# Kernel tuning notes

Measured on AMD Instinct MI355X. Metric: run time of the kernel, lower is better.

The kernel has to match this reference:

```python
import jax, jax.numpy as jnp
import numpy as np
from jax import lax

B, S, C_IN, D, H, P, W, DFF, K = 32, 4096, 32, 256, 8, 24, 64, 512, 5
DH = D // H
EPS = 1e-5


def _make_starts():
    stride = max(1, W // 2)
    idx = list(range(0, max(S - W + 1, 1), stride))
    if len(idx) == 0 or idx[-1] != S - W:
        if S - W >= 0:
            idx.append(S - W)
    return np.asarray(idx)

STARTS = _make_starts()                      # [M]
WIDX = STARTS[:, None] + np.arange(W)        # [M, W] patch gather indices


def setup_inputs() -> dict:
    key = jax.random.key(0)
    ks = jax.random.split(key, 24)
    r = lambda i, shape, s=0.02: (jax.random.normal(ks[i], shape, jnp.float32) * s)
    return {
        "x": jax.random.normal(ks[0], (B, S, C_IN), jnp.float32),
        "last_close_unused": jnp.zeros((B,), jnp.float32),
        "dw_w": r(1, (C_IN, 1, K), 0.2),      # depthwise conv kernel
        "pw_w": r(2, (D, C_IN), 0.1),         # pointwise conv (1x1)
        "bn_g": jnp.ones((D,), jnp.float32),
        "bn_b": jnp.zeros((D,), jnp.float32),
        "lg_Wq": r(3, (D, D)), "lg_Wk": r(4, (D, D)),
        "lg_Wv": r(5, (D, D)), "lg_Wo": r(6, (D, D)),
        "dec_Qd": r(7, (P, D), 1.0 / np.sqrt(D)),
        "dec_Wq": r(8, (D, D)), "dec_Wk": r(9, (D, D)),
        "dec_Wv": r(10, (D, D)), "dec_Wo": r(11, (D, D)),
        "ff1_w": r(12, (DFF, D)), "ff1_b": jnp.zeros((DFF,), jnp.float32),
        "ff2_w": r(13, (D, DFF)), "ff2_b": jnp.zeros((D,), jnp.float32),
        "out_w": r(14, (1, D)), "out_b": jnp.zeros((1,), jnp.float32),
        "gate_logits": jnp.tile(jnp.array([0.2, 0.4, 0.4], jnp.float32), (P, 1)),
    }


def _ln(x):
    m = x.mean(-1, keepdims=True)
    v = ((x - m) ** 2).mean(-1, keepdims=True)
    return (x - m) / jnp.sqrt(v + EPS)


def _split(t):  # [B, L, D] -> [B, H, L, DH]
    return t.reshape(t.shape[0], -1, H, DH).transpose(0, 2, 1, 3)


def _mha(Q, KV, Wq, Wk, Wv, scale):
    q = _split(Q @ Wq.T)
    k = _split(KV @ Wk.T)
    v = _split(KV @ Wv.T)
    attn = jax.nn.softmax(jnp.einsum('bhqd,bhkd->bhqk', q, k) * scale, axis=-1)
    o = jnp.einsum('bhqk,bhkd->bhqd', attn, v)
    o = o.transpose(0, 2, 1, 3).reshape(Q.shape[0], -1, D)
    return o, attn


def reference(x, last_close_unused, dw_w, pw_w, bn_g, bn_b,
              lg_Wq, lg_Wk, lg_Wv, lg_Wo,
              dec_Qd, dec_Wq, dec_Wk, dec_Wv, dec_Wo,
              ff1_w, ff1_b, ff2_w, ff2_b, out_w, out_b, gate_logits):
    # --- DepthwisePointwise front-end ---
    xt = jnp.transpose(x, (0, 2, 1))                         # [B, C, S]
    z = lax.conv_general_dilated(xt, dw_w, (1,), [(K // 2, K // 2)],
                                 dimension_numbers=('NCH', 'OIH', 'NCH'),
                                 feature_group_count=C_IN)
    z = jnp.einsum('dc,bcs->bds', pw_w, z)                   # pointwise 1x1
    z = jax.nn.gelu(z, approximate=False)
    m = z.mean((0, 2), keepdims=True)                        # BatchNorm1d (batch stats)
    v = ((z - m) ** 2).mean((0, 2), keepdims=True)
    z = (z - m) / jnp.sqrt(v + EPS) * bn_g[None, :, None] + bn_b[None, :, None]
    z = jnp.transpose(z, (0, 2, 1))                          # [B, S, D]

    # --- LocalGlobalAttention: patch-mean queries over full sequence K/V ---
    Q = z[:, WIDX].mean(axis=2)                              # [B, M, D]
    scale = 1.0 / np.sqrt(DH)
    o, attn_g = _mha(Q, z, lg_Wq, lg_Wk, lg_Wv, scale)
    Hh = _ln(o @ lg_Wo.T + Q)                                # [B, M, D]

    # --- CrossDecoder: learned queries ---
    Qd = jnp.broadcast_to(dec_Qd[None], (B, P, D))
    o2, attn_d = _mha(Qd, Hh, dec_Wq, dec_Wk, dec_Wv, scale)
    z2 = _ln(o2 @ dec_Wo.T + Qd)
    u = jax.nn.gelu(z2 @ ff1_w.T + ff1_b, approximate=False)
    u = _ln(u @ ff2_w.T + ff2_b + z2)
    y_global = (u @ out_w.T + out_b)[..., 0]                 # [B, P]

    # --- Gated combine: residual=0, local=global ---
    g = jax.nn.softmax(gate_logits, axis=-1)                 # [P, 3]
    y = g[:, 1][None, :] * y_global + g[:, 2][None, :] * y_global
    return (y, attn_g, attn_d)
```

## Files before the change

kernel.cpp:

```cpp
#include <hip/hip_runtime.h>
#include <hip/hip_bf16.h>

typedef unsigned short u16;
typedef __attribute__((ext_vector_type(4))) float f32x4;
typedef __attribute__((ext_vector_type(8))) short s16x8;

__device__ __forceinline__ float b2f(u16 u) { return __uint_as_float(((unsigned)u) << 16); }
__device__ __forceinline__ u16 f2b(float f) {
    unsigned u = __float_as_uint(f);
    unsigned r = (u + 0x7fffu + ((u >> 16) & 1u)) >> 16;
    return (u16)r;
}
__device__ __forceinline__ float gelu_f(float x) {
    return 0.5f * x * (1.0f + erff(x * 0.70710678118654752f));
}

__global__ __launch_bounds__(256) void dw_k(const float* __restrict__ x,
        const float* __restrict__ dw_w, u16* __restrict__ z1b)
{
    int g = blockIdx.x * 256 + threadIdx.x;
    int c = g & 31, grp = g >> 5;
    int b = grp >> 9, s8 = (grp & 511) << 3;
    float wv[5];
    #pragma unroll
    for (int k = 0; k < 5; ++k) wv[k] = dw_w[c * 5 + k];
    const float* xb = x + ((size_t)b * 4096 + s8) * 32 + c;
    float xv[12];
    #pragma unroll
    for (int i = 0; i < 12; ++i) {
        int s = s8 + i - 2;
        xv[i] = (s >= 0 && s < 4096) ? xb[(i - 2) * 32] : 0.0f;
    }
    u16* zb = z1b + ((size_t)b * 4096 + s8) * 32 + c;
    #pragma unroll
    for (int j = 0; j < 8; ++j) {
        float acc = 0;
        #pragma unroll
        for (int k = 0; k < 5; ++k) acc += xv[j + k] * wv[k];
        zb[j * 32] = f2b(acc);
    }
}

__global__ __launch_bounds__(256) void prep0_k(const float* __restrict__ pw_w,
        const float* __restrict__ lg_Wq, const float* __restrict__ lg_Wo,
        const float* __restrict__ dec_Wk, const float* __restrict__ dec_Wv,
        const float* __restrict__ dec_Wo, const float* __restrict__ ff1_w,
        const float* __restrict__ ff2_w,
        u16* __restrict__ pwb, u16* __restrict__ Wq_b, u16* __restrict__ Wo_b,
        u16* __restrict__ Wk2_b, u16* __restrict__ Wv2_b, u16* __restrict__ Wo2b,
        u16* __restrict__ ff1b, u16* __restrict__ ff2b)
{
    int idx = blockIdx.x * 256 + threadIdx.x;
    if (idx < 327680) {
        int which = idx >> 16, r = idx & 65535;
        const float* srcs[5] = {lg_Wq, lg_Wo, dec_Wk, dec_Wv, dec_Wo};
        u16* dsts[5] = {Wq_b, Wo_b, Wk2_b, Wv2_b, Wo2b};
        dsts[which][r] = f2b(srcs[which][r]);
    } else if (idx < 458752) {
        int r = idx - 327680;
        ff1b[r] = f2b(ff1_w[r]);
    } else if (idx < 589824) {
        int r = idx - 458752;
        ff2b[r] = f2b(ff2_w[r]);
    } else {
        int r = idx - 589824;
        pwb[r] = f2b(pw_w[r]);
    }
}

__global__ __launch_bounds__(256) void pw_k(const u16* __restrict__ z1b,
        const u16* __restrict__ pwb, u16* __restrict__ zp,
        float* __restrict__ csum, float* __restrict__ csum2)
{
    __shared__ u16 As[64][32];
    const int t = threadIdx.x;
    const int r0 = blockIdx.x * 64;
    const int lane = t & 63, w = t >> 6;
    const int l16 = lane & 15, hi = lane >> 4;

    {
        int row = t >> 2, seg = t & 3;
        *(s16x8*)&As[row][seg * 8] = *(const s16x8*)(z1b + (size_t)(r0 + row) * 32 + seg * 8);
    }
    __syncthreads();

    const int n0 = w * 64;
    f32x4 zero = {0, 0, 0, 0};
    s16x8 bf[4];
    #pragma unroll
    for (int ni = 0; ni < 4; ++ni)
        bf[ni] = *(const s16x8*)(pwb + (n0 + ni * 16 + l16) * 32 + hi * 8);

    float cl[4] = {0,0,0,0}, ch[4] = {0,0,0,0};
    float ql[4] = {0,0,0,0}, qh[4] = {0,0,0,0};

    #pragma unroll
    for (int mi = 0; mi < 4; ++mi) {
        s16x8 af = *(const s16x8*)&As[mi * 16 + l16][hi * 8];
        #pragma unroll
        for (int ni = 0; ni < 4; ++ni) {
            f32x4 acc = __builtin_amdgcn_mfma_f32_16x16x32_bf16(af, bf[ni], zero, 0, 0, 0);
            int col = n0 + ni * 16 + l16;
            int rowb = r0 + mi * 16 + hi * 4;
            #pragma unroll
            for (int r = 0; r < 4; ++r) {
                float e = gelu_f(acc[r]);
                zp[(size_t)(rowb + r) * 256 + col] = f2b(e);
                if (mi < 2) { cl[ni] += e; ql[ni] += e * e; }
                else        { ch[ni] += e; qh[ni] += e * e; }
            }
        }
    }
    #pragma unroll
    for (int ni = 0; ni < 4; ++ni) {
        #pragma unroll
        for (int m = 16; m <= 32; m <<= 1) {
            cl[ni] += __shfl_xor(cl[ni], m);
            ch[ni] += __shfl_xor(ch[ni], m);
            ql[ni] += __shfl_xor(ql[ni], m);
            qh[ni] += __shfl_xor(qh[ni], m);
        }
        if (lane < 16) {
            int col = n0 + ni * 16 + lane;
            size_t bc = (size_t)(r0 >> 5);
            csum [bc * 256 + col]       = cl[ni];
            csum [(bc + 1) * 256 + col] = ch[ni];
            csum2[bc * 256 + col]       = ql[ni];
            csum2[(bc + 1) * 256 + col] = qh[ni];
        }
    }
}

__global__ __launch_bounds__(256) void stats2_k(const float* __restrict__ csum,
        const float* __restrict__ csum2, float* __restrict__ statp)
{
    int j = blockIdx.x, t = threadIdx.x;
    float s1 = 0, s2 = 0;
    for (int i = 0; i < 64; ++i) {
        s1 += csum [(size_t)(j * 64 + i) * 256 + t];
        s2 += csum2[(size_t)(j * 64 + i) * 256 + t];
    }
    statp[j * 512 + t] = s1;
    statp[j * 512 + 256 + t] = s2;
}

__global__ __launch_bounds__(256) void prep1_k(const float* __restrict__ statp,
        const float* __restrict__ bn_g, const float* __restrict__ bn_b,
        const float* __restrict__ gate_logits,
        float* __restrict__ a_ws, float* __restrict__ c_ws, float* __restrict__ coef)
{
    int t = threadIdx.x;
    float s1 = 0, s2 = 0;
    for (int j = 0; j < 64; ++j) {
        s1 += statp[j * 512 + t];
        s2 += statp[j * 512 + 256 + t];
    }
    const float invN = 1.0f / 131072.0f;
    float mean = s1 * invN;
    float var = s2 * invN - mean * mean;
    float av = bn_g[t] * rsqrtf(var + 1e-5f);
    a_ws[t] = av;
    c_ws[t] = bn_b[t] - mean * av;
    if (t < 24) {
        float g0 = gate_logits[t * 3], g1 = gate_logits[t * 3 + 1], g2 = gate_logits[t * 3 + 2];
        float mx = fmaxf(g0, fmaxf(g1, g2));
        float e0 = __expf(g0 - mx), e1 = __expf(g1 - mx), e2 = __expf(g2 - mx);
        coef[t] = (e1 + e2) / (e0 + e1 + e2);
    }
}

__global__ __launch_bounds__(256) void prep2b_k(const float* __restrict__ lg_Wk,
        const float* __restrict__ lg_Wv, const float* __restrict__ a_ws,
        const float* __restrict__ c_ws,
        u16* __restrict__ Wk_b, u16* __restrict__ Wv_b,
        float* __restrict__ betak, float* __restrict__ betav)
{
    __shared__ float red[4];
    int bid = blockIdx.x;
    int which = bid >> 8, row = bid & 255, t = threadIdx.x;
    const float* Wsrc = which ? lg_Wv : lg_Wk;
    float wv = Wsrc[row * 256 + t];
    (which ? Wv_b : Wk_b)[row * 256 + t] = f2b(wv * a_ws[t]);
    float v = wv * c_ws[t];
    for (int m = 32; m; m >>= 1) v += __shfl_xor(v, m);
    if ((t & 63) == 0) red[t >> 6] = v;
    __syncthreads();
    if (t == 0) (which ? betav : betak)[row] = red[0] + red[1] + red[2] + red[3];
}

__global__ __launch_bounds__(256) void q2_k(const float* __restrict__ dec_Qd,
        const float* __restrict__ dec_Wq, float* __restrict__ q2)
{
    __shared__ float wq[16][260];
    __shared__ float qd[24][260];
    int j = blockIdx.x, t = threadIdx.x;
    for (int idx = t; idx < 4096; idx += 256) {
        int tl = idx >> 8, d = idx & 255;
        wq[tl][d] = dec_Wq[(j * 16 + tl) * 256 + d];
    }
    for (int idx = t; idx < 6144; idx += 256) {
        int p = idx >> 8, d = idx & 255;
        qd[p][d] = dec_Qd[idx];
    }
    __syncthreads();
    for (int o = t; o < 384; o += 256) {
        int p = o >> 4, tl = o & 15;
        float s = 0;
        #pragma unroll 8
        for (int d = 0; d < 256; ++d) s += qd[p][d] * wq[tl][d];
        q2[p * 256 + j * 16 + tl] = s;
    }
}

__global__ __launch_bounds__(256) void qfinal_k(const float* __restrict__ csum,
        const float* __restrict__ a_ws, const float* __restrict__ c_ws,
        float* __restrict__ Qf, u16* __restrict__ Qb)
{
    int bid = blockIdx.x;
    int m = bid & 127, t = threadIdx.x;
    float val = 0.0f;
    if (m < 127) {
        float c0 = csum[(size_t)bid * 256 + t];
        float c1 = csum[(size_t)(bid + 1) * 256 + t];
        val = (c0 + c1) * (1.0f / 64.0f) * a_ws[t] + c_ws[t];
    }
    Qf[(size_t)bid * 256 + t] = val;
    Qb[(size_t)bid * 256 + t] = f2b(val);
}

__global__ __launch_bounds__(256) void kv_k(const u16* __restrict__ zp,
        const u16* __restrict__ Wk, const u16* __restrict__ Wv,
        const float* __restrict__ betak, const float* __restrict__ betav,
        u16* __restrict__ kb, u16* __restrict__ vT)
{
    __shared__ u16 As[64 * 256];
    const int t = threadIdx.x;
    const int r0 = blockIdx.x * 64;
    const int lane = t & 63, w = t >> 6;
    const int l16 = lane & 15, hi = lane >> 4;

    const u16* Ag = zp + (size_t)r0 * 256;
    #pragma unroll
    for (int i = 0; i < 8; ++i) {
        int c = t + i * 256;
        int row = c >> 5, c16 = c & 31;
        s16x8 v = *(const s16x8*)(Ag + row * 256 + c16 * 8);
        int boff = (c16 * 16) ^ ((row & 7) << 4);
        *(s16x8*)((char*)As + row * 512 + boff) = v;
    }
    __syncthreads();

    const int n0 = w * 64;
    f32x4 zero = {0, 0, 0, 0};
    f32x4 acc[4][4];
    #pragma unroll
    for (int mi = 0; mi < 4; ++mi)
        #pragma unroll
        for (int ni = 0; ni < 4; ++ni) acc[mi][ni] = zero;

    #pragma unroll
    for (int kk = 0; kk < 8; ++kk) {
        s16x8 af[4], bfk[4];
        #pragma unroll
        for (int mi = 0; mi < 4; ++mi) {
            int row = mi * 16 + l16;
            int boff = (kk * 64 + hi * 16) ^ ((row & 7) << 4);
            af[mi] = *(const s16x8*)((const char*)As + row * 512 + boff);
        }
        #pragma unroll
        for (int ni = 0; ni < 4; ++ni)
            bfk[ni] = *(const s16x8*)(Wk + (n0 + ni * 16 + l16) * 256 + kk * 32 + hi * 8);
        #pragma unroll
        for (int mi = 0; mi < 4; ++mi)
            #pragma unroll
            for (int ni = 0; ni < 4; ++ni)
                acc[mi][ni] = __builtin_amdgcn_mfma_f32_16x16x32_bf16(af[mi], bfk[ni], acc[mi][ni], 0, 0, 0);
    }
    #pragma unroll
    for (int mi = 0; mi < 4; ++mi) {
        #pragma unroll
        for (int ni = 0; ni < 4; ++ni) {
            int col = n0 + ni * 16 + l16;
            float bv = betak[col];
            int rowb = r0 + mi * 16 + hi * 4;
            #pragma unroll
            for (int r = 0; r < 4; ++r)
                kb[(size_t)(rowb + r) * 256 + col] = f2b(acc[mi][ni][r] + bv);
        }
    }
    #pragma unroll
    for (int mi = 0; mi < 4; ++mi)
        #pragma unroll
        for (int ni = 0; ni < 4; ++ni) acc[mi][ni] = zero;
    #pragma unroll
    for (int kk = 0; kk < 8; ++kk) {
        s16x8 af[4], bfv[4];
        #pragma unroll
        for (int mi = 0; mi < 4; ++mi) {
            int row = mi * 16 + l16;
            int boff = (kk * 64 + hi * 16) ^ ((row & 7) << 4);
            af[mi] = *(const s16x8*)((const char*)As + row * 512 + boff);
        }
        #pragma unroll
        for (int ni = 0; ni < 4; ++ni)
            bfv[ni] = *(const s16x8*)(Wv + (n0 + ni * 16 + l16) * 256 + kk * 32 + hi * 8);
        #pragma unroll
        for (int mi = 0; mi < 4; ++mi)
            #pragma unroll
            for (int ni = 0; ni < 4; ++ni)
                acc[mi][ni] = __builtin_amdgcn_mfma_f32_16x16x32_bf16(af[mi], bfv[ni], acc[mi][ni], 0, 0, 0);
    }
    const int b = r0 >> 12, sbase = r0 & 4095;
    #pragma unroll
    for (int mi = 0; mi < 4; ++mi) {
        #pragma unroll
        for (int ni = 0; ni < 4; ++ni) {
            int col = n0 + ni * 16 + l16;
            float bv = betav[col];
            int h = col >> 5, dh = col & 31;
            int s = sbase + mi * 16 + hi * 4;
            ushort4 pk;
            pk.x = f2b(acc[mi][ni][0] + bv);
            pk.y = f2b(acc[mi][ni][1] + bv);
            pk.z = f2b(acc[mi][ni][2] + bv);
            pk.w = f2b(acc[mi][ni][3] + bv);
            *(ushort4*)(vT + ((size_t)((b * 8 + h) * 32 + dh)) * 4096 + s) = pk;
        }
    }
}

template<int MODE>
__global__ __launch_bounds__(256) void gemm_g(const u16* __restrict__ A,
        const u16* __restrict__ W, const float* __restrict__ bias,
        void* __restrict__ Cout, int K, int ntn)
{
    __shared__ u16 As[64 * 256];
    const int t = threadIdx.x;
    const int rt = blockIdx.x / ntn, nt = blockIdx.x % ntn;
    const int r0 = rt * 64, N = ntn * 256;
    const int lane = t & 63, w = t >> 6;
    const int l16 = lane & 15, hi = lane >> 4;

    const u16* Ag = A + (size_t)r0 * K;
    const int n0 = w * 64;
    f32x4 zero = {0, 0, 0, 0};
    f32x4 acc[4][4];
    #pragma unroll
    for (int mi = 0; mi < 4; ++mi)
        #pragma unroll
        for (int ni = 0; ni < 4; ++ni) acc[mi][ni] = zero;

    for (int kc = 0; kc < K; kc += 256) {
        if (kc) __syncthreads();
        #pragma unroll
        for (int i = 0; i < 8; ++i) {
            int c = t + i * 256;
            int row = c >> 5, c16 = c & 31;
            s16x8 v = *(const s16x8*)(Ag + (size_t)row * K + kc + c16 * 8);
            int boff = (c16 * 16) ^ ((row & 7) << 4);
            *(s16x8*)((char*)As + row * 512 + boff) = v;
        }
        __syncthreads();
        #pragma unroll
        for (int kk = 0; kk < 8; ++kk) {
            s16x8 af[4], bf[4];
            #pragma unroll
            for (int mi = 0; mi < 4; ++mi) {
                int row = mi * 16 + l16;
                int boff = (kk * 64 + hi * 16) ^ ((row & 7) << 4);
                af[mi] = *(const s16x8*)((const char*)As + row * 512 + boff);
            }
            #pragma unroll
            for (int ni = 0; ni < 4; ++ni) {
                int j = nt * 256 + n0 + ni * 16 + l16;
                bf[ni] = *(const s16x8*)(W + (size_t)j * K + kc + kk * 32 + hi * 8);
            }
            #pragma unroll
            for (int mi = 0; mi < 4; ++mi)
                #pragma unroll
                for (int ni = 0; ni < 4; ++ni)
                    acc[mi][ni] = __builtin_amdgcn_mfma_f32_16x16x32_bf16(af[mi], bf[ni], acc[mi][ni], 0, 0, 0);
        }
    }

    #pragma unroll
    for (int mi = 0; mi < 4; ++mi) {
        #pragma unroll
        for (int ni = 0; ni < 4; ++ni) {
            int col = nt * 256 + n0 + ni * 16 + l16;
            float bv = bias ? bias[col] : 0.0f;
            int rowb = r0 + mi * 16 + hi * 4;
            #pragma unroll
            for (int r = 0; r < 4; ++r) {
                float v = acc[mi][ni][r] + bv;
                if (MODE == 0)      ((u16*)Cout)[(size_t)(rowb + r) * N + col] = f2b(v);
                else if (MODE == 1) ((float*)Cout)[(size_t)(rowb + r) * N + col] = v;
                else                ((u16*)Cout)[(size_t)(rowb + r) * N + col] = f2b(gelu_f(v));
            }
        }
    }
}

__global__ __launch_bounds__(512) void attn_p1(const u16* __restrict__ qb,
        const u16* __restrict__ kb, const u16* __restrict__ vT,
        float* __restrict__ den, float* __restrict__ o_part)
{
    const int bid = blockIdx.x;
    const int b = bid >> 6, h = (bid >> 3) & 7, chunk = bid & 7;
    const int t = threadIdx.x, w = t >> 6, lane = t & 63;
    const int l16 = lane & 15, hi = lane >> 4;
    const float scale = 0.17677669529663687f;

    __shared__ u16 p_lds[8][16][48];

    s16x8 qf = *(const s16x8*)(qb + ((size_t)(b * 128 + w * 16 + l16)) * 256 + h * 32 + hi * 8);
    const u16* kbase = kb + (size_t)b * 4096 * 256 + h * 32 + hi * 8;
    const u16* vbase = vT + ((size_t)(b * 8 + h)) * 32 * 4096 + hi * 8;

    float dacc[4] = {0, 0, 0, 0};
    f32x4 zero = {0, 0, 0, 0};
    f32x4 oacc[2]; oacc[0] = zero; oacc[1] = zero;

    const int sbeg = chunk * 512, send = sbeg + 512;
    for (int s0 = sbeg; s0 < send; s0 += 32) {
        #pragma unroll
        for (int sub = 0; sub < 2; ++sub) {
            int sg = s0 + sub * 16 + l16;
            s16x8 kf = *(const s16x8*)(kbase + (size_t)sg * 256);
            f32x4 lg = __builtin_amdgcn_mfma_f32_16x16x32_bf16(qf, kf, zero, 0, 0, 0);
            #pragma unroll
            for (int r = 0; r < 4; ++r) {
                float e = __expf(lg[r] * scale);
                dacc[r] += e;
                p_lds[w][hi * 4 + r][sub * 16 + l16] = f2b(e);
            }
        }
        s16x8 pf = *(const s16x8*)(&p_lds[w][l16][hi * 8]);
        #pragma unroll
        for (int vi = 0; vi < 2; ++vi) {
            s16x8 vf = *(const s16x8*)(vbase + ((size_t)(vi * 16 + l16)) * 4096 + s0);
            oacc[vi] = __builtin_amdgcn_mfma_f32_16x16x32_bf16(pf, vf, oacc[vi], 0, 0, 0);
        }
    }

    #pragma unroll
    for (int m = 1; m <= 8; m <<= 1) {
        #pragma unroll
        for (int r = 0; r < 4; ++r) dacc[r] += __shfl_xor(dacc[r], m);
    }
    if (l16 == 0) {
        #pragma unroll
        for (int r = 0; r < 4; ++r)
            den[(size_t)chunk * 32768 + (b * 8 + h) * 128 + w * 16 + hi * 4 + r] = dacc[r];
    }
    #pragma unroll
    for (int vi = 0; vi < 2; ++vi) {
        #pragma unroll
        for (int r = 0; r < 4; ++r) {
            int mg = w * 16 + hi * 4 + r;
            o_part[(size_t)chunk * 1048576 + (size_t)(b * 128 + mg) * 256 + h * 32 + vi * 16 + l16] = oacc[vi][r];
        }
    }
}

__global__ __launch_bounds__(256) void dinv_k(const float* __restrict__ den, float* __restrict__ den_inv)
{
    int i = blockIdx.x * 256 + threadIdx.x;
    float s = 0;
    #pragma unroll
    for (int c = 0; c < 8; ++c) s += den[(size_t)c * 32768 + i];
    den_inv[i] = 1.0f / s;
}

__global__ __launch_bounds__(256) void norm_k(const float* __restrict__ o_part,
        const float* __restrict__ den_inv, u16* __restrict__ ob)
{
    size_t idx = (size_t)blockIdx.x * 256 + threadIdx.x;
    int row = (int)(idx >> 8);
    int col = (int)(idx & 255);
    int b = row >> 7, m = row & 127, h = col >> 5;
    float s = 0;
    #pragma unroll
    for (int c = 0; c < 8; ++c) s += o_part[(size_t)c * 1048576 + idx];
    ob[idx] = f2b(s * den_inv[b * 1024 + h * 128 + m]);
}

__global__ __launch_bounds__(512) void attn_p2(const u16* __restrict__ qb,
        const u16* __restrict__ kb, const float* __restrict__ den_inv,
        float* __restrict__ attn_out)
{
    const int bid = blockIdx.x;
    const int b = bid >> 6, h = (bid >> 3) & 7, chunk = bid & 7;
    const int t = threadIdx.x, w = t >> 6, lane = t & 63;
    const int l16 = lane & 15, hi = lane >> 4;
    const float scale = 0.17677669529663687f;

    __shared__ float buf[8][16][68];

    s16x8 qf = *(const s16x8*)(qb + ((size_t)(b * 128 + w * 16 + l16)) * 256 + h * 32 + hi * 8);
    const u16* kbase = kb + (size_t)b * 4096 * 256 + h * 32 + hi * 8;

    float rinv[4];
    #pragma unroll
    for (int r = 0; r < 4; ++r)
        rinv[r] = den_inv[b * 1024 + h * 128 + w * 16 + hi * 4 + r];

    f32x4 zero = {0, 0, 0, 0};
    float* ab = attn_out + (size_t)(b * 8 + h) * 127 * 4096;
    const int nrow = (w < 7) ? 16 : 15;

    const int sbeg = chunk * 512, send = sbeg + 512;
    for (int s0 = sbeg; s0 < send; s0 += 64) {
        #pragma unroll
        for (int kk = 0; kk < 4; ++kk) {
            int sg = s0 + kk * 16 + l16;
            s16x8 kf = *(const s16x8*)(kbase + (size_t)sg * 256);
            f32x4 lg = __builtin_amdgcn_mfma_f32_16x16x32_bf16(qf, kf, zero, 0, 0, 0);
            #pragma unroll
            for (int r = 0; r < 4; ++r)
                buf[w][hi * 4 + r][kk * 16 + l16] = __expf(lg[r] * scale) * rinv[r];
        }
        float* dst = ab + (size_t)(w * 16) * 4096 + s0 + lane;
        for (int r = 0; r < nrow; ++r)
            dst[(size_t)r * 4096] = buf[w][r][lane];
    }
}

__global__ __launch_bounds__(256) void ln_hh(const float* __restrict__ og,
        const float* __restrict__ Qf, u16* __restrict__ Hb)
{
    __shared__ float red[8];
    int row = blockIdx.x, t = threadIdx.x;
    float v = og[(size_t)row * 256 + t] + Qf[(size_t)row * 256 + t];
    float s = v;
    for (int m = 32; m; m >>= 1) s += __shfl_xor(s, m);
    if ((t & 63) == 0) red[t >> 6] = s;
    __syncthreads();
    float mean = (red[0] + red[1] + red[2] + red[3]) * (1.0f / 256.0f);
    __syncthreads();
    float d = v - mean;
    float q = d * d;
    for (int m = 32; m; m >>= 1) q += __shfl_xor(q, m);
    if ((t & 63) == 0) red[t >> 6] = q;
    __syncthreads();
    float var = (red[0] + red[1] + red[2] + red[3]) * (1.0f / 256.0f);
    Hb[(size_t)row * 256 + t] = f2b(d * rsqrtf(var + 1e-5f));
}

__global__ __launch_bounds__(256) void dec_attn_k(const float* __restrict__ q2,
        const u16* __restrict__ k2b, const u16* __restrict__ v2b,
        float* __restrict__ attn_d, u16* __restrict__ o2b)
{
    __shared__ float qs2[24 * 32];
    __shared__ float ks[128][33];
    __shared__ float vs[128][33];
    __shared__ float lg2[24 * 128];
    __shared__ float sinv[24];
    int bid = blockIdx.x, b = bid >> 3, h = bid & 7;
    int t = threadIdx.x;
    const float scale = 0.17677669529663687f;
    for (int idx = t; idx < 4096; idx += 256) {
        int row = idx >> 5, c = idx & 31;
        ks[row][c] = b2f(k2b[((size_t)(b * 128 + row)) * 256 + h * 32 + c]);
        vs[row][c] = b2f(v2b[((size_t)(b * 128 + row)) * 256 + h * 32 + c]);
    }
    for (int idx = t; idx < 768; idx += 256) {
        int p = idx >> 5, i = idx & 31;
        qs2[idx] = q2[p * 256 + h * 32 + i];
    }
    __syncthreads();
    for (int idx = t; idx < 3048; idx += 256) {
        int p = idx / 127, m = idx - p * 127;
        float s = 0;
        #pragma unroll 8
        for (int i = 0; i < 32; ++i) s += qs2[p * 32 + i] * ks[m][i];
        lg2[p * 128 + m] = __expf(s * scale);
    }
    __syncthreads();
    if (t < 24) {
        float s = 0;
        for (int m = 0; m < 127; ++m) s += lg2[t * 128 + m];
        sinv[t] = 1.0f / s;
    }
    __syncthreads();
    float* ad = attn_d + (size_t)bid * 24 * 127;
    for (int idx = t; idx < 3048; idx += 256) {
        int p = idx / 127, m = idx - p * 127;
        float av = lg2[p * 128 + m] * sinv[p];
        lg2[p * 128 + m] = av;
        ad[idx] = av;
    }
    __syncthreads();
    for (int idx = t; idx < 768; idx += 256) {
        int p = idx >> 5, dh = idx & 31;
        float s = 0;
        for (int m = 0; m < 127; ++m)
            s += lg2[p * 128 + m] * vs[m][dh];
        o2b[((size_t)(b * 24 + p)) * 256 + h * 32 + dh] = f2b(s);
    }
}

__global__ __launch_bounds__(256) void ln3_k(const float* __restrict__ og2,
        const float* __restrict__ dec_Qd, float* __restrict__ z2f, u16* __restrict__ z2b)
{
    __shared__ float red[8];
    int row = blockIdx.x, p = row % 24, t = threadIdx.x;
    float v = og2[(size_t)row * 256 + t] + dec_Qd[p * 256 + t];
    float s = v;
    for (int m = 32; m; m >>= 1) s += __shfl_xor(s, m);
    if ((t & 63) == 0) red[t >> 6] = s;
    __syncthreads();
    float mean = (red[0] + red[1] + red[2] + red[3]) * (1.0f / 256.0f);
    __syncthreads();
    float d = v - mean, q = d * d;
    for (int m = 32; m; m >>= 1) q += __shfl_xor(q, m);
    if ((t & 63) == 0) red[t >> 6] = q;
    __syncthreads();
    float var = (red[0] + red[1] + red[2] + red[3]) * (1.0f / 256.0f);
    float u = d * rsqrtf(var + 1e-5f);
    z2f[(size_t)row * 256 + t] = u;
    z2b[(size_t)row * 256 + t] = f2b(u);
}

__global__ __launch_bounds__(256) void ln5_k(const float* __restrict__ uraw,
        const float* __restrict__ z2f, const float* __restrict__ out_w,
        const float* __restrict__ out_b, const float* __restrict__ coef,
        float* __restrict__ y)
{
    __shared__ float red[8];
    int row = blockIdx.x, p = row % 24, t = threadIdx.x;
    float v = uraw[(size_t)row * 256 + t] + z2f[(size_t)row * 256 + t];
    float s = v;
    for (int m = 32; m; m >>= 1) s += __shfl_xor(s, m);
    if ((t & 63) == 0) red[t >> 6] = s;
    __syncthreads();
    float mean = (red[0] + red[1] + red[2] + red[3]) * (1.0f / 256.0f);
    __syncthreads();
    float d = v - mean, q = d * d;
    for (int m = 32; m; m >>= 1) q += __shfl_xor(q, m);
    if ((t & 63) == 0) red[t >> 6] = q;
    __syncthreads();
    float var = (red[0] + red[1] + red[2] + red[3]) * (1.0f / 256.0f);
    float u = d * rsqrtf(var + 1e-5f);
    __syncthreads();
    float yp = u * out_w[t];
    for (int m = 32; m; m >>= 1) yp += __shfl_xor(yp, m);
    if ((t & 63) == 0) red[t >> 6] = yp;
    __syncthreads();
    if (t == 0) {
        float tot = red[0] + red[1] + red[2] + red[3] + out_b[0];
        y[row] = coef[p] * tot;
    }
}

extern "C" void kernel_launch(void* const* d_in, const int* in_sizes, int n_in,
                              void* d_out, int out_size, void* d_ws, size_t ws_size,
                              hipStream_t stream)
{
    const float* x        = (const float*)d_in[0];
    const float* dw_w     = (const float*)d_in[2];
    const float* pw_w     = (const float*)d_in[3];
    const float* bn_g     = (const float*)d_in[4];
    const float* bn_b     = (const float*)d_in[5];
    const float* lg_Wq    = (const float*)d_in[6];
    const float* lg_Wk    = (const float*)d_in[7];
    const float* lg_Wv    = (const float*)d_in[8];
    const float* lg_Wo    = (const float*)d_in[9];
    const float* dec_Qd   = (const float*)d_in[10];
    const float* dec_Wq   = (const float*)d_in[11];
    const float* dec_Wk   = (const float*)d_in[12];
    const float* dec_Wv   = (const float*)d_in[13];
    const float* dec_Wo   = (const float*)d_in[14];
    const float* ff1_w    = (const float*)d_in[15];
    const float* ff1_b    = (const float*)d_in[16];
    const float* ff2_w    = (const float*)d_in[17];
    const float* ff2_b    = (const float*)d_in[18];
    const float* out_w    = (const float*)d_in[19];
    const float* out_b    = (const float*)d_in[20];
    const float* gate_lg  = (const float*)d_in[21];

    char* ws = (char*)d_ws;
    size_t off = 0;
    auto alloc = [&](size_t bytes) -> void* {
        void* p = ws + off;
        off = (off + bytes + 255) & ~(size_t)255;
        return p;
    };
    u16*   zp    = (u16*)  alloc(67108864);
    u16*   kb    = (u16*)  alloc(67108864);
    u16*   vT    = (u16*)  alloc(67108864);
    u16*   z1b   = (u16*)  alloc(8388608);
    float* csum  = (float*)alloc(4194304);
    float* csum2 = (float*)alloc(4194304);
    float* Qf    = (float*)alloc(4194304);
    u16*   Qb    = (u16*)  alloc(2097152);
    u16*   qb    = (u16*)  alloc(2097152);
    u16*   ob    = (u16*)  alloc(2097152);
    float* og    = (float*)alloc(4194304);
    u16*   Hb    = (u16*)  alloc(2097152);
    u16*   k2b   = (u16*)  alloc(2097152);
    u16*   v2b   = (u16*)  alloc(2097152);
    float* o_part= (float*)alloc(33554432);
    u16*   o2b   = (u16*)  alloc(393216);
    float* og2   = (float*)alloc(786432);
    float* z2f   = (float*)alloc(786432);
    u16*   z2b   = (u16*)  alloc(393216);
    u16*   u1b   = (u16*)  alloc(786432);
    float* uraw  = (float*)alloc(786432);
    float* q2    = (float*)alloc(24576);
    float* den   = (float*)alloc(1048576);
    float* den_i = (float*)alloc(131072);
    float* statp = (float*)alloc(131072);
    float* a_ws  = (float*)alloc(1024);
    float* c_ws  = (float*)alloc(1024);
    float* betak = (float*)alloc(1024);
    float* betav = (float*)alloc(1024);
    float* coef  = (float*)alloc(256);
    u16*   pwb   = (u16*)  alloc(16384);
    u16*   Wk_b  = (u16*)  alloc(131072);
    u16*   Wv_b  = (u16*)  alloc(131072);
    u16*   Wq_b  = (u16*)  alloc(131072);
    u16*   Wo_b  = (u16*)  alloc(131072);
    u16*   Wk2_b = (u16*)  alloc(131072);
    u16*   Wv2_b = (u16*)  alloc(131072);
    u16*   Wo2b  = (u16*)  alloc(131072);
    u16*   ff1b  = (u16*)  alloc(262144);
    u16*   ff2b  = (u16*)  alloc(262144);

    float* y_out  = (float*)d_out;
    float* attn_g = y_out + 768;
    float* attn_d = attn_g + (size_t)32 * 8 * 127 * 4096;

    dw_k<<<2048, 256, 0, stream>>>(x, dw_w, z1b);
    prep0_k<<<2336, 256, 0, stream>>>(pw_w, lg_Wq, lg_Wo, dec_Wk, dec_Wv, dec_Wo, ff1_w, ff2_w,
                                      pwb, Wq_b, Wo_b, Wk2_b, Wv2_b, Wo2b, ff1b, ff2b);
    pw_k<<<2048, 256, 0, stream>>>(z1b, pwb, zp, csum, csum2);
    stats2_k<<<64, 256, 0, stream>>>(csum, csum2, statp);
    prep1_k<<<1, 256, 0, stream>>>(statp, bn_g, bn_b, gate_lg, a_ws, c_ws, coef);
    prep2b_k<<<512, 256, 0, stream>>>(lg_Wk, lg_Wv, a_ws, c_ws, Wk_b, Wv_b, betak, betav);
    q2_k<<<16, 256, 0, stream>>>(dec_Qd, dec_Wq, q2);
    qfinal_k<<<4096, 256, 0, stream>>>(csum, a_ws, c_ws, Qf, Qb);
    kv_k<<<2048, 256, 0, stream>>>(zp, Wk_b, Wv_b, betak, betav, kb, vT);
    gemm_g<0><<<64, 256, 0, stream>>>(Qb, Wq_b, nullptr, qb, 256, 1);
    attn_p1<<<2048, 512, 0, stream>>>(qb, kb, vT, den, o_part);
    dinv_k<<<128, 256, 0, stream>>>(den, den_i);
    norm_k<<<4096, 256, 0, stream>>>(o_part, den_i, ob);
    attn_p2<<<2048, 512, 0, stream>>>(qb, kb, den_i, attn_g);
    gemm_g<1><<<64, 256, 0, stream>>>(ob, Wo_b, nullptr, og, 256, 1);
    ln_hh<<<4096, 256, 0, stream>>>(og, Qf, Hb);
    gemm_g<0><<<64, 256, 0, stream>>>(Hb, Wk2_b, nullptr, k2b, 256, 1);
    gemm_g<0><<<64, 256, 0, stream>>>(Hb, Wv2_b, nullptr, v2b, 256, 1);
    dec_attn_k<<<256, 256, 0, stream>>>(q2, k2b, v2b, attn_d, o2b);
    gemm_g<1><<<12, 256, 0, stream>>>(o2b, Wo2b, nullptr, og2, 256, 1);
    ln3_k<<<768, 256, 0, stream>>>(og2, dec_Qd, z2f, z2b);
    gemm_g<2><<<24, 256, 0, stream>>>(z2b, ff1b, ff1_b, u1b, 256, 2);
    gemm_g<1><<<12, 256, 0, stream>>>(u1b, ff2b, ff2_b, uraw, 512, 1);
    ln5_k<<<768, 256, 0, stream>>>(uraw, z2f, out_w, out_b, coef, y_out);
}
```

Before: 560.7 us.

## Fuse depthwise into pointwise conv, fuse Q build into Q GEMM, prefetch attention K/V

Merges the depthwise conv into the pointwise conv kernel via a shared-memory halo tile, which drops the z1b intermediate buffer. It also folds the patch-mean Q construction into the Q projection GEMM with the softmax scale times log2(e) pre-applied, so attention can use exp2f. Other changes: the Q residual is recomputed inside ln_hh, the K2/V2 GEMMs are merged into one launch, and the attention loop software-prefetches the next K/V fragments. The goal is fewer launches and less intermediate traffic, at the cost of rounding Q to bf16 with the scale already folded in.

New measurement: 554.6 us, median of 2. Within noise of the previous version (-1.1%).

```diff
diff --git a/kernel.cpp b/kernel.cpp
--- a/kernel.cpp
+++ b/kernel.cpp
@@ -1,5 +1,6 @@
 #include <hip/hip_runtime.h>
 #include <hip/hip_bf16.h>
+#include <cmath>
 
 typedef unsigned short u16;
 typedef __attribute__((ext_vector_type(4))) float f32x4;
@@ -15,31 +16,7 @@
     return 0.5f * x * (1.0f + erff(x * 0.70710678118654752f));
 }
 
-__global__ __launch_bounds__(256) void dw_k(const float* __restrict__ x,
-        const float* __restrict__ dw_w, u16* __restrict__ z1b)
-{
-    int g = blockIdx.x * 256 + threadIdx.x;
-    int c = g & 31, grp = g >> 5;
-    int b = grp >> 9, s8 = (grp & 511) << 3;
-    float wv[5];
-    #pragma unroll
-    for (int k = 0; k < 5; ++k) wv[k] = dw_w[c * 5 + k];
-    const float* xb = x + ((size_t)b * 4096 + s8) * 32 + c;
-    float xv[12];
-    #pragma unroll
-    for (int i = 0; i < 12; ++i) {
-        int s = s8 + i - 2;
-        xv[i] = (s >= 0 && s < 4096) ? xb[(i - 2) * 32] : 0.0f;
-    }
-    u16* zb = z1b + ((size_t)b * 4096 + s8) * 32 + c;
-    #pragma unroll
-    for (int j = 0; j < 8; ++j) {
-        float acc = 0;
-        #pragma unroll
-        for (int k = 0; k < 5; ++k) acc += xv[j + k] * wv[k];
-        zb[j * 32] = f2b(acc);
-    }
-}
+#define FOLD 0.25503590f
 
 __global__ __launch_bounds__(256) void prep0_k(const float* __restrict__ pw_w,
         const float* __restrict__ lg_Wq, const float* __restrict__ lg_Wo,
@@ -68,19 +45,35 @@
     }
 }
 
-__global__ __launch_bounds__(256) void pw_k(const u16* __restrict__ z1b,
-        const u16* __restrict__ pwb, u16* __restrict__ zp,
-        float* __restrict__ csum, float* __restrict__ csum2)
-{
-    __shared__ u16 As[64][32];
+__global__ __launch_bounds__(256) void dwpw_k(const float* __restrict__ x,
+        const float* __restrict__ dw_w, const u16* __restrict__ pwb,
+        u16* __restrict__ zp, float* __restrict__ csum, float* __restrict__ csum2)
+{
+    __shared__ float xs[68][33];
+    __shared__ __align__(16) u16 As[64][40];
     const int t = threadIdx.x;
+    const int b = blockIdx.x >> 6, s0 = (blockIdx.x & 63) << 6;
     const int r0 = blockIdx.x * 64;
     const int lane = t & 63, w = t >> 6;
     const int l16 = lane & 15, hi = lane >> 4;
 
-    {
-        int row = t >> 2, seg = t & 3;
-        *(s16x8*)&As[row][seg * 8] = *(const s16x8*)(z1b + (size_t)(r0 + row) * 32 + seg * 8);
+    for (int idx = t; idx < 68 * 32; idx += 256) {
+        int row = idx >> 5, c = idx & 31;
+        int sg = s0 - 2 + row;
+        xs[row][c] = (sg >= 0 && sg < 4096) ? x[((size_t)b * 4096 + sg) * 32 + c] : 0.0f;
+    }
+    const int cc = t & 31;
+    float wv[5];
+    #pragma unroll
+    for (int k = 0; k < 5; ++k) wv[k] = dw_w[cc * 5 + k];
+    __syncthreads();
+    #pragma unroll
+    for (int i = 0; i < 8; ++i) {
+        int sl = (t + i * 256) >> 5;
+        float acc = 0;
+        #pragma unroll
+        for (int k = 0; k < 5; ++k) acc += xs[sl + k][cc] * wv[k];
+        As[sl][cc] = f2b(acc);
     }
     __syncthreads();
 
@@ -212,20 +205,81 @@
     }
 }
 
-__global__ __launch_bounds__(256) void qfinal_k(const float* __restrict__ csum,
+__global__ __launch_bounds__(256) void qgemm_k(const float* __restrict__ csum,
         const float* __restrict__ a_ws, const float* __restrict__ c_ws,
-        float* __restrict__ Qf, u16* __restrict__ Qb)
-{
-    int bid = blockIdx.x;
-    int m = bid & 127, t = threadIdx.x;
-    float val = 0.0f;
-    if (m < 127) {
-        float c0 = csum[(size_t)bid * 256 + t];
-        float c1 = csum[(size_t)(bid + 1) * 256 + t];
-        val = (c0 + c1) * (1.0f / 64.0f) * a_ws[t] + c_ws[t];
-    }
-    Qf[(size_t)bid * 256 + t] = val;
-    Qb[(size_t)bid * 256 + t] = f2b(val);
+        const u16* __restrict__ W, u16* __restrict__ qb)
+{
+    __shared__ u16 As[64 * 256];
+    __shared__ float aa[256], ccx[256];
+    const int t = threadIdx.x;
+    const int r0 = blockIdx.x * 64;
+    const int lane = t & 63, w = t >> 6;
+    const int l16 = lane & 15, hi = lane >> 4;
+
+    aa[t] = a_ws[t] * 0.015625f;
+    ccx[t] = c_ws[t];
+    __syncthreads();
+
+    #pragma unroll
+    for (int i = 0; i < 8; ++i) {
+        int c = t + i * 256;
+        int row = c >> 5, c16 = c & 31;
+        int g = r0 + row, mm = g & 127;
+        u16 tmp[8];
+        if (mm == 127) {
+            #pragma unroll
+            for (int j = 0; j < 8; ++j) tmp[j] = 0;
+        } else {
+            const float* c0p = csum + (size_t)g * 256 + c16 * 8;
+            const float* c1p = c0p + 256;
+            #pragma unroll
+            for (int j = 0; j < 8; ++j) {
+                int d = c16 * 8 + j;
+                tmp[j] = f2b((c0p[j] + c1p[j]) * aa[d] + ccx[d]);
+            }
+        }
+        int boff = (c16 * 16) ^ ((row & 7) << 4);
+        *(s16x8*)((char*)As + row * 512 + boff) = *(s16x8*)tmp;
+    }
+    __syncthreads();
+
+    const int n0 = w * 64;
+    f32x4 zero = {0, 0, 0, 0};
+    f32x4 acc[4][4];
+    #pragma unroll
+    for (int mi = 0; mi < 4; ++mi)
+        #pragma unroll
+        for (int ni = 0; ni < 4; ++ni) acc[mi][ni] = zero;
+
+    #pragma unroll
+    for (int kk = 0; kk < 8; ++kk) {
+        s16x8 af[4], bf[4];
+        #pragma unroll
+        for (int mi = 0; mi < 4; ++mi) {
+            int row = mi * 16 + l16;
+            int boff = (kk * 64 + hi * 16) ^ ((row & 7) << 4);
+            af[mi] = *(const s16x8*)((const char*)As + row * 512 + boff);
+        }
+        #pragma unroll
+        for (int ni = 0; ni < 4; ++ni)
+            bf[ni] = *(const s16x8*)(W + (n0 + ni * 16 + l16) * 256 + kk * 32 + hi * 8);
+        #pragma unroll
+        for (int mi = 0; mi < 4; ++mi)
+            #pragma unroll
+            for (int ni = 0; ni < 4; ++ni)
+                acc[mi][ni] = __builtin_amdgcn_mfma_f32_16x16x32_bf16(af[mi], bf[ni], acc[mi][ni], 0, 0, 0);
+    }
+
+    #pragma unroll
+    for (int mi = 0; mi < 4; ++mi)
+        #pragma unroll
+        for (int ni = 0; ni < 4; ++ni) {
+            int col = n0 + ni * 16 + l16;
+            int rowb = r0 + mi * 16 + hi * 4;
+            #pragma unroll
+            for (int r = 0; r < 4; ++r)
+                qb[(size_t)(rowb + r) * 256 + col] = f2b(acc[mi][ni][r] * FOLD);
+        }
 }
 
 __global__ __launch_bounds__(256) void kv_k(const u16* __restrict__ zp,
@@ -277,7 +331,7 @@
                 acc[mi][ni] = __builtin_amdgcn_mfma_f32_16x16x32_bf16(af[mi], bfk[ni], acc[mi][ni], 0, 0, 0);
     }
     #pragma unroll
-    for (int mi = 0; mi < 4; ++mi) {
+    for (int mi = 0; mi < 4; ++mi)
         #pragma unroll
         for (int ni = 0; ni < 4; ++ni) {
             int col = n0 + ni * 16 + l16;
@@ -287,7 +341,7 @@
             for (int r = 0; r < 4; ++r)
                 kb[(size_t)(rowb + r) * 256 + col] = f2b(acc[mi][ni][r] + bv);
         }
-    }
+
     #pragma unroll
     for (int mi = 0; mi < 4; ++mi)
         #pragma unroll
@@ -312,7 +366,7 @@
     }
     const int b = r0 >> 12, sbase = r0 & 4095;
     #pragma unroll
-    for (int mi = 0; mi < 4; ++mi) {
+    for (int mi = 0; mi < 4; ++mi)
         #pragma unroll
         for (int ni = 0; ni < 4; ++ni) {
             int col = n0 + ni * 16 + l16;
@@ -326,7 +380,6 @@
             pk.w = f2b(acc[mi][ni][3] + bv);
             *(ushort4*)(vT + ((size_t)((b * 8 + h) * 32 + dh)) * 4096 + s) = pk;
         }
-    }
 }
 
 template<int MODE>
@@ -384,7 +437,7 @@
     }
 
     #pragma unroll
-    for (int mi = 0; mi < 4; ++mi) {
+    for (int mi = 0; mi < 4; ++mi)
         #pragma unroll
         for (int ni = 0; ni < 4; ++ni) {
             int col = nt * 256 + n0 + ni * 16 + l16;
@@ -398,7 +451,68 @@
                 else                ((u16*)Cout)[(size_t)(rowb + r) * N + col] = f2b(gelu_f(v));
             }
         }
-    }
+}
+
+__global__ __launch_bounds__(256) void gemm_dual(const u16* __restrict__ A,
+        const u16* __restrict__ W0, const u16* __restrict__ W1,
+        u16* __restrict__ C0, u16* __restrict__ C1)
+{
+    __shared__ u16 As[64 * 256];
+    const int t = threadIdx.x;
+    const int which = blockIdx.x >> 6;
+    const int r0 = (blockIdx.x & 63) * 64;
+    const u16* W = which ? W1 : W0;
+    u16* C = which ? C1 : C0;
+    const int lane = t & 63, w = t >> 6;
+    const int l16 = lane & 15, hi = lane >> 4;
+
+    const u16* Ag = A + (size_t)r0 * 256;
+    #pragma unroll
+    for (int i = 0; i < 8; ++i) {
+        int c = t + i * 256;
+        int row = c >> 5, c16 = c & 31;
+        s16x8 v = *(const s16x8*)(Ag + row * 256 + c16 * 8);
+        int boff = (c16 * 16) ^ ((row & 7) << 4);
+        *(s16x8*)((char*)As + row * 512 + boff) = v;
+    }
+    __syncthreads();
+
+    const int n0 = w * 64;
+    f32x4 zero = {0, 0, 0, 0};
+    f32x4 acc[4][4];
+    #pragma unroll
+    for (int mi = 0; mi < 4; ++mi)
+        #pragma unroll
+        for (int ni = 0; ni < 4; ++ni) acc[mi][ni] = zero;
+
+    #pragma unroll
+    for (int kk = 0; kk < 8; ++kk) {
+        s16x8 af[4], bf[4];
+        #pragma unroll
+        for (int mi = 0; mi < 4; ++mi) {
+            int row = mi * 16 + l16;
+            int boff = (kk * 64 + hi * 16) ^ ((row & 7) << 4);
+            af[mi] = *(const s16x8*)((const char*)As + row * 512 + boff);
+        }
+        #pragma unroll
+        for (int ni = 0; ni < 4; ++ni)
+            bf[ni] = *(const s16x8*)(W + (n0 + ni * 16 + l16) * 256 + kk * 32 + hi * 8);
+        #pragma unroll
+        for (int mi = 0; mi < 4; ++mi)
+            #pragma unroll
+            for (int ni = 0; ni < 4; ++ni)
+                acc[mi][ni] = __builtin_amdgcn_mfma_f32_16x16x32_bf16(af[mi], bf[ni], acc[mi][ni], 0, 0, 0);
+    }
+    #pragma unroll
+    for (int mi = 0; mi < 4; ++mi)
+        #pragma unroll
+        for (int ni = 0; ni < 4; ++ni) {
+            int col = n0 + ni * 16 + l16;
+            int rowb = r0 + mi * 16 + hi * 4;
+            #pragma unroll
+            for (int r = 0; r < 4; ++r)
+                C[(size_t)(rowb + r) * 256 + col] = f2b(acc[mi][ni][r]);
+        }
 }
 
 __global__ __launch_bounds__(512) void attn_p1(const u16* __restrict__ qb,
@@ -409,7 +523,6 @@
     const int b = bid >> 6, h = (bid >> 3) & 7, chunk = bid & 7;
     const int t = threadIdx.x, w = t >> 6, lane = t & 63;
     const int l16 = lane & 15, hi = lane >> 4;
-    const float scale = 0.17677669529663687f;
 
     __shared__ u16 p_lds[8][16][48];
 
@@ -422,25 +535,33 @@
     f32x4 oacc[2]; oacc[0] = zero; oacc[1] = zero;
 
     const int sbeg = chunk * 512, send = sbeg + 512;
+    s16x8 kf0 = *(const s16x8*)(kbase + (size_t)(sbeg + l16) * 256);
+    s16x8 kf1 = *(const s16x8*)(kbase + (size_t)(sbeg + 16 + l16) * 256);
+    s16x8 vf0 = *(const s16x8*)(vbase + ((size_t)l16) * 4096 + sbeg);
+    s16x8 vf1 = *(const s16x8*)(vbase + ((size_t)(16 + l16)) * 4096 + sbeg);
+
     for (int s0 = sbeg; s0 < send; s0 += 32) {
-        #pragma unroll
-        for (int sub = 0; sub < 2; ++sub) {
-            int sg = s0 + sub * 16 + l16;
-            s16x8 kf = *(const s16x8*)(kbase + (size_t)sg * 256);
-            f32x4 lg = __builtin_amdgcn_mfma_f32_16x16x32_bf16(qf, kf, zero, 0, 0, 0);
-            #pragma unroll
-            for (int r = 0; r < 4; ++r) {
-                float e = __expf(lg[r] * scale);
-                dacc[r] += e;
-                p_lds[w][hi * 4 + r][sub * 16 + l16] = f2b(e);
-            }
+        s16x8 k0 = kf0, k1 = kf1, v0 = vf0, v1 = vf1;
+        int sn = s0 + 32;
+        if (sn < send) {
+            kf0 = *(const s16x8*)(kbase + (size_t)(sn + l16) * 256);
+            kf1 = *(const s16x8*)(kbase + (size_t)(sn + 16 + l16) * 256);
+            vf0 = *(const s16x8*)(vbase + ((size_t)l16) * 4096 + sn);
+            vf1 = *(const s16x8*)(vbase + ((size_t)(16 + l16)) * 4096 + sn);
+        }
+        f32x4 lg0 = __builtin_amdgcn_mfma_f32_16x16x32_bf16(qf, k0, zero, 0, 0, 0);
+        f32x4 lg1 = __builtin_amdgcn_mfma_f32_16x16x32_bf16(qf, k1, zero, 0, 0, 0);
+        #pragma unroll
+        for (int r = 0; r < 4; ++r) {
+            float e0 = exp2f(lg0[r]);
+            float e1 = exp2f(lg1[r]);
+            dacc[r] += e0 + e1;
+            p_lds[w][hi * 4 + r][l16] = f2b(e0);
+            p_lds[w][hi * 4 + r][16 + l16] = f2b(e1);
         }
         s16x8 pf = *(const s16x8*)(&p_lds[w][l16][hi * 8]);
-        #pragma unroll
-        for (int vi = 0; vi < 2; ++vi) {
-            s16x8 vf = *(const s16x8*)(vbase + ((size_t)(vi * 16 + l16)) * 4096 + s0);
-            oacc[vi] = __builtin_amdgcn_mfma_f32_16x16x32_bf16(pf, vf, oacc[vi], 0, 0, 0);
-        }
+        oacc[0] = __builtin_amdgcn_mfma_f32_16x16x32_bf16(pf, v0, oacc[0], 0, 0, 0);
+        oacc[1] = __builtin_amdgcn_mfma_f32_16x16x32_bf16(pf, v1, oacc[1], 0, 0, 0);
     }
 
     #pragma unroll
@@ -454,13 +575,12 @@
             den[(size_t)chunk * 32768 + (b * 8 + h) * 128 + w * 16 + hi * 4 + r] = dacc[r];
     }
     #pragma unroll
-    for (int vi = 0; vi < 2; ++vi) {
+    for (int vi = 0; vi < 2; ++vi)
         #pragma unroll
         for (int r = 0; r < 4; ++r) {
             int mg = w * 16 + hi * 4 + r;
             o_part[(size_t)chunk * 1048576 + (size_t)(b * 128 + mg) * 256 + h * 32 + vi * 16 + l16] = oacc[vi][r];
         }
-    }
 }
 
 __global__ __launch_bounds__(256) void dinv_k(const float* __restrict__ den, float* __restrict__ den_inv)
@@ -493,7 +613,6 @@
     const int b = bid >> 6, h = (bid >> 3) & 7, chunk = bid & 7;
     const int t = threadIdx.x, w = t >> 6, lane = t & 63;
     const int l16 = lane & 15, hi = lane >> 4;
-    const float scale = 0.17677669529663687f;
 
     __shared__ float buf[8][16][68];
 
@@ -518,7 +637,7 @@
             f32x4 lg = __builtin_amdgcn_mfma_f32_16x16x32_bf16(qf, kf, zero, 0, 0, 0);
             #pragma unroll
             for (int r = 0; r < 4; ++r)
-                buf[w][hi * 4 + r][kk * 16 + l16] = __expf(lg[r] * scale) * rinv[r];
+                buf[w][hi * 4 + r][kk * 16 + l16] = exp2f(lg[r]) * rinv[r];
         }
         float* dst = ab + (size_t)(w * 16) * 4096 + s0 + lane;
         for (int r = 0; r < nrow; ++r)
@@ -527,11 +646,17 @@
 }
 
 __global__ __launch_bounds__(256) void ln_hh(const float* __restrict__ og,
-        const float* __restrict__ Qf, u16* __restrict__ Hb)
+        const float* __restrict__ csum, const float* __restrict__ a_ws,
+        const float* __restrict__ c_ws, u16* __restrict__ Hb)
 {
     __shared__ float red[8];
     int row = blockIdx.x, t = threadIdx.x;
-    float v = og[(size_t)row * 256 + t] + Qf[(size_t)row * 256 + t];
+    int mm = row & 127;
+    float qv = 0.0f;
+    if (mm != 127)
+        qv = (csum[(size_t)row * 256 + t] + csum[(size_t)(row + 1) * 256 + t]) *
+             (0.015625f * a_ws[t]) + c_ws[t];
+    float v = og[(size_t)row * 256 + t] + qv;
     float s = v;
     for (int m = 32; m; m >>= 1) s += __shfl_xor(s, m);
     if ((t & 63) == 0) red[t >> 6] = s;
@@ -689,11 +814,8 @@
     u16*   zp    = (u16*)  alloc(67108864);
     u16*   kb    = (u16*)  alloc(67108864);
     u16*   vT    = (u16*)  alloc(67108864);
-    u16*   z1b   = (u16*)  alloc(8388608);
     float* csum  = (float*)alloc(4194304);
     float* csum2 = (float*)alloc(4194304);
-    float* Qf    = (float*)alloc(4194304);
-    u16*   Qb    = (u16*)  alloc(2097152);
     u16*   qb    = (u16*)  alloc(2097152);
     u16*   ob    = (u16*)  alloc(2097152);
     float* og    = (float*)alloc(4194304);
@@ -731,25 +853,22 @@
     float* attn_g = y_out + 768;
     float* attn_d = attn_g + (size_t)32 * 8 * 127 * 4096;
 
-    dw_k<<<2048, 256, 0, stream>>>(x, dw_w, z1b);
     prep0_k<<<2336, 256, 0, stream>>>(pw_w, lg_Wq, lg_Wo, dec_Wk, dec_Wv, dec_Wo, ff1_w, ff2_w,
                                       pwb, Wq_b, Wo_b, Wk2_b, Wv2_b, Wo2b, ff1b, ff2b);
-    pw_k<<<2048, 256, 0, stream>>>(z1b, pwb, zp, csum, csum2);
+    dwpw_k<<<2048, 256, 0, stream>>>(x, dw_w, pwb, zp, csum, csum2);
     stats2_k<<<64, 256, 0, stream>>>(csum, csum2, statp);
     prep1_k<<<1, 256, 0, stream>>>(statp, bn_g, bn_b, gate_lg, a_ws, c_ws, coef);
     prep2b_k<<<512, 256, 0, stream>>>(lg_Wk, lg_Wv, a_ws, c_ws, Wk_b, Wv_b, betak, betav);
     q2_k<<<16, 256, 0, stream>>>(dec_Qd, dec_Wq, q2);
-    qfinal_k<<<4096, 256, 0, stream>>>(csum, a_ws, c_ws, Qf, Qb);
+    qgemm_k<<<64, 256, 0, stream>>>(csum, a_ws, c_ws, Wq_b, qb);
     kv_k<<<2048, 256, 0, stream>>>(zp, Wk_b, Wv_b, betak, betav, kb, vT);
-    gemm_g<0><<<64, 256, 0, stream>>>(Qb, Wq_b, nullptr, qb, 256, 1);
     attn_p1<<<2048, 512, 0, stream>>>(qb, kb, vT, den, o_part);
     dinv_k<<<128, 256, 0, stream>>>(den, den_i);
     norm_k<<<4096, 256, 0, stream>>>(o_part, den_i, ob);
     attn_p2<<<2048, 512, 0, stream>>>(qb, kb, den_i, attn_g);
     gemm_g<1><<<64, 256, 0, stream>>>(ob, Wo_b, nullptr, og, 256, 1);
-    ln_hh<<<4096, 256, 0, stream>>>(og, Qf, Hb);
-    gemm_g<0><<<64, 256, 0, stream>>>(Hb, Wk2_b, nullptr, k2b, 256, 1);
-    gemm_g<0><<<64, 256, 0, stream>>>(Hb, Wv2_b, nullptr, v2b, 256, 1);
+    ln_hh<<<4096, 256, 0, stream>>>(og, csum, a_ws, c_ws, Hb);
+    gemm_dual<<<128, 256, 0, stream>>>(Hb, Wk2_b, Wv2_b, k2b, v2b);
     dec_attn_k<<<256, 256, 0, stream>>>(q2, k2b, v2b, attn_d, o2b);
     gemm_g<1><<<12, 256, 0, stream>>>(o2b, Wo2b, nullptr, og2, 256, 1);
     ln3_k<<<768, 256, 0, stream>>>(og2, dec_Qd, z2f, z2b);
```
